# Optimization experiments

Measured on AMD Instinct MI355X. Metric: run time of the kernel, lower is better.

The kernel has to match this reference:

```python
import jax, jax.numpy as jnp
import numpy as np

N_NODES = 50000
N_EDGES = 400000
DIM = 64
HEADS = 8
NUM_GRAPHS = 64
OUT_DIM = 32
NEG_SLOPE = 0.2
EPS = 1e-5


def setup_inputs() -> dict:
    key = jax.random.key(0)
    ks = jax.random.split(key, 20)
    inp = {
        "x": jax.random.normal(ks[0], (N_NODES, DIM), dtype=jnp.float32),
        "edge_index": jax.random.randint(ks[1], (2, N_EDGES), 0, N_NODES, dtype=jnp.int64),
        "batch": jnp.sort(jax.random.randint(ks[2], (N_NODES,), 0, NUM_GRAPHS, dtype=jnp.int64)),
    }
    s = 0.05
    # GATConv layer 1 (in=DIM, out=DIM per head, heads=HEADS, concat=False)
    inp["W1"] = jax.random.normal(ks[3], (DIM, HEADS * DIM), dtype=jnp.float32) * s
    inp["a_src1"] = jax.random.normal(ks[4], (HEADS, DIM), dtype=jnp.float32) * s
    inp["a_dst1"] = jax.random.normal(ks[5], (HEADS, DIM), dtype=jnp.float32) * s
    inp["b1"] = jnp.zeros((DIM,), dtype=jnp.float32)
    inp["ln1_w"] = jnp.ones((DIM,), dtype=jnp.float32)
    inp["ln1_b"] = jnp.zeros((DIM,), dtype=jnp.float32)
    # GATConv layer 2
    inp["W2"] = jax.random.normal(ks[6], (DIM, HEADS * DIM), dtype=jnp.float32) * s
    inp["a_src2"] = jax.random.normal(ks[7], (HEADS, DIM), dtype=jnp.float32) * s
    inp["a_dst2"] = jax.random.normal(ks[8], (HEADS, DIM), dtype=jnp.float32) * s
    inp["b2"] = jnp.zeros((DIM,), dtype=jnp.float32)
    inp["ln2_w"] = jnp.ones((DIM,), dtype=jnp.float32)
    inp["ln2_b"] = jnp.zeros((DIM,), dtype=jnp.float32)
    # DownStream head
    inp["Wh"] = jax.random.normal(ks[9], (DIM, OUT_DIM), dtype=jnp.float32) * s
    inp["bh"] = jnp.zeros((OUT_DIM,), dtype=jnp.float32)
    return inp


def _edge_softmax(logits, dst, n):
    # per-destination-node softmax over incoming edges; logits: [E, H]
    m = jax.ops.segment_max(logits, dst, num_segments=n)
    e = jnp.exp(logits - m[dst])
    s = jax.ops.segment_sum(e, dst, num_segments=n)
    return e / (s[dst] + 1e-16)


def _gat_conv(x, src, dst, W, a_src, a_dst, b):
    # PyG GATConv, heads=HEADS, concat=False (mean over heads), eval mode (no dropout)
    n = x.shape[0]
    h = (x @ W).reshape(n, HEADS, -1)              # [N, H, D]
    al_s = jnp.einsum("nhd,hd->nh", h, a_src)      # [N, H]
    al_d = jnp.einsum("nhd,hd->nh", h, a_dst)
    logits = jax.nn.leaky_relu(al_s[src] + al_d[dst], NEG_SLOPE)  # [E, H]
    alpha = _edge_softmax(logits, dst, n)
    out = jax.ops.segment_sum(alpha[:, :, None] * h[src], dst, num_segments=n)  # [N, H, D]
    return out.mean(axis=1) + b


def _graph_layer_norm(x, batch, w, b):
    # PyG LayerNorm mode='graph': normalize over all nodes and channels of each graph
    f = x.shape[1]
    cnt = jax.ops.segment_sum(jnp.ones((x.shape[0],), x.dtype), batch, num_segments=NUM_GRAPHS)
    norm = jnp.clip(cnt, 1.0) * f
    mean = jax.ops.segment_sum(x.sum(axis=-1), batch, num_segments=NUM_GRAPHS) / norm
    xc = x - mean[batch][:, None]
    var = jax.ops.segment_sum((xc * xc).sum(axis=-1), batch, num_segments=NUM_GRAPHS) / norm
    out = xc * jax.lax.rsqrt(var + EPS)[batch][:, None]
    return out * w + b


def reference(x, edge_index, batch, W1, a_src1, a_dst1, b1, ln1_w, ln1_b,
              W2, a_src2, a_dst2, b2, ln2_w, ln2_b, Wh, bh):
    n = x.shape[0]
    loops = jnp.arange(n, dtype=edge_index.dtype)
    src = jnp.concatenate([edge_index[0], loops])   # add_self_loops (PyG default)
    dst = jnp.concatenate([edge_index[1], loops])

    # My_GATConv (dropout is identity in eval)
    h = x + _gat_conv(x, src, dst, W1, a_src1, a_dst1, b1)
    h = jax.nn.relu(_graph_layer_norm(h, batch, ln1_w, ln1_b))
    h = h + _gat_conv(h, src, dst, W2, a_src2, a_dst2, b2)
    h = jax.nn.relu(_graph_layer_norm(h, batch, ln2_w, ln2_b))

    # global_mean_pool over batch
    cnt = jax.ops.segment_sum(jnp.ones((n,), h.dtype), batch, num_segments=NUM_GRAPHS)
    pooled = jax.ops.segment_sum(h, batch, num_segments=NUM_GRAPHS) / jnp.clip(cnt, 1.0)[:, None]

    # DownStream head
    return jax.nn.relu(pooled @ Wh + bh)
```

## Files before the change

kernel.cpp:

```cpp
#include <hip/hip_runtime.h>
#include <math.h>

#define N_NODES 50000
#define N_EDGES 400000
#define E_TOT   (N_EDGES + N_NODES)
#define NG      64
#define NEG_SLOPE 0.2f

typedef __attribute__((ext_vector_type(8))) short bf16x8;
typedef __attribute__((ext_vector_type(4))) float f32x4;

__device__ __forceinline__ float lrelu(float x){ return x > 0.f ? x : NEG_SLOPE * x; }
__device__ __forceinline__ ushort f2bf(float f){
  union { float f; unsigned u; } v; v.f = f;
  unsigned r = v.u + 0x7FFFu + ((v.u >> 16) & 1u);
  return (ushort)(r >> 16);
}
__device__ __forceinline__ float bf2f(ushort u){
  return __uint_as_float(((unsigned)u) << 16);
}
__device__ __forceinline__ float bflo(unsigned u){ return __uint_as_float(u << 16); }
__device__ __forceinline__ float bfhi(unsigned u){ return __uint_as_float(u & 0xffff0000u); }

__device__ __forceinline__ void acc8(float* acc, uint4 w, float xv){
  acc[0] = fmaf(bflo(w.x), xv, acc[0]);
  acc[1] = fmaf(bfhi(w.x), xv, acc[1]);
  acc[2] = fmaf(bflo(w.y), xv, acc[2]);
  acc[3] = fmaf(bfhi(w.y), xv, acc[3]);
  acc[4] = fmaf(bflo(w.z), xv, acc[4]);
  acc[5] = fmaf(bfhi(w.z), xv, acc[5]);
  acc[6] = fmaf(bflo(w.w), xv, acc[6]);
  acc[7] = fmaf(bfhi(w.w), xv, acc[7]);
}

#define SETUP_PREP   (2048 + 2 * 32768)
#define SETUP_BOUNDS (SETUP_PREP + N_NODES + 1)
#define SETUP_TOTAL  (SETUP_BOUNDS + E_TOT)

__global__ void setup_kernel(const float* __restrict__ W1, const float* __restrict__ as1,
                             const float* __restrict__ ad1, const float* __restrict__ W2,
                             const float* __restrict__ as2, const float* __restrict__ ad2,
                             const int* __restrict__ batch, const int* __restrict__ ei,
                             float* __restrict__ wa1, float* __restrict__ wa2,
                             ushort* __restrict__ w1pT, ushort* __restrict__ w2pT,
                             int* __restrict__ gstart, int* __restrict__ counts){
  int idx = blockIdx.x * blockDim.x + threadIdx.x;
  if (idx < 2048){
    const float* W = (idx < 1024) ? W1 : W2;
    const float* asr = (idx < 1024) ? as1 : as2;
    const float* adr = (idx < 1024) ? ad1 : ad2;
    float* wa = (idx < 1024) ? wa1 : wa2;
    int i = idx & 1023;
    int k = i >> 4, c = i & 15;
    int h = c & 7;
    const float* a = (c < 8) ? asr : adr;
    float s = 0.f;
#pragma unroll
    for (int d = 0; d < 64; ++d) s = fmaf(W[k * 512 + h * 64 + d], a[h * 64 + d], s);
    wa[i] = s;
  } else if (idx < SETUP_PREP){
    int i = idx - 2048;
    const float* W = (i < 32768) ? W1 : W2;
    ushort* wpT = (i < 32768) ? w1pT : w2pT;
    i &= 32767;
    int j = i >> 9, k = i & 511;
    int h = k >> 6, d = k & 63;
    wpT[i] = f2bf(W[d * 512 + h * 64 + j] * 0.125f);
  } else if (idx < SETUP_BOUNDS){
    int n = idx - SETUP_PREP;
    int g = (n < N_NODES) ? batch[n] : NG;
    if (n == 0){
      for (int gg = 0; gg <= g; ++gg) gstart[gg] = 0;
    } else {
      int gp = batch[n - 1];
      for (int gg = gp + 1; gg <= g; ++gg) gstart[gg] = n;
    }
  } else if (idx < SETUP_TOTAL){
    int e = idx - SETUP_BOUNDS;
    int dst = (e < N_EDGES) ? ei[N_EDGES + e] : (e - N_EDGES);
    atomicAdd(&counts[dst], 1);
  }
}

#define SCAN_B 1024
#define SCAN_NB ((N_NODES + SCAN_B - 1) / SCAN_B)

__global__ __launch_bounds__(SCAN_B) void scan1_kernel(const int* __restrict__ counts,
                                                       int* __restrict__ row_off,
                                                       int* __restrict__ blocksum){
  __shared__ int sh[SCAN_B];
  int i = blockIdx.x * SCAN_B + threadIdx.x;
  int v = (i < N_NODES) ? counts[i] : 0;
  sh[threadIdx.x] = v;
  __syncthreads();
#pragma unroll
  for (int off = 1; off < SCAN_B; off <<= 1){
    int add = (threadIdx.x >= (unsigned)off) ? sh[threadIdx.x - off] : 0;
    __syncthreads();
    sh[threadIdx.x] += add;
    __syncthreads();
  }
  if (i < N_NODES) row_off[i] = sh[threadIdx.x] - v;
  if (threadIdx.x == SCAN_B - 1) blocksum[blockIdx.x] = sh[SCAN_B - 1];
}

__global__ void scan2_kernel(int* __restrict__ blocksum, int* __restrict__ blockoff){
  __shared__ int sh[64];
  int t = threadIdx.x;
  int v = (t < SCAN_NB) ? blocksum[t] : 0;
  sh[t] = v;
  __syncthreads();
#pragma unroll
  for (int off = 1; off < 64; off <<= 1){
    int add = (t >= off) ? sh[t - off] : 0;
    __syncthreads();
    sh[t] += add;
    __syncthreads();
  }
  if (t < SCAN_NB) blockoff[t] = sh[t] - v;
  if (t == 63) blockoff[SCAN_NB] = sh[63];
}

__global__ void scan3_kernel(int* __restrict__ row_off, const int* __restrict__ blockoff){
  int i = blockIdx.x * blockDim.x + threadIdx.x;
  if (i < N_NODES) row_off[i] += blockoff[i >> 10];
  if (i == 0) row_off[N_NODES] = blockoff[SCAN_NB];
}

__global__ void scatter_kernel(const int* __restrict__ ei, const int* __restrict__ row_off,
                               int* __restrict__ cursor, int* __restrict__ csr_src){
  int e = blockIdx.x * blockDim.x + threadIdx.x;
  if (e >= E_TOT) return;
  int src, dst;
  if (e < N_EDGES){ src = ei[e]; dst = ei[N_EDGES + e]; }
  else            { src = dst = e - N_EDGES; }
  int pos = row_off[dst] + atomicAdd(&cursor[dst], 1);
  csr_src[pos] = src;
}

__global__ void al1_kernel(const float* __restrict__ xin, const float* __restrict__ wa,
                           float* __restrict__ al, ushort* __restrict__ xbf){
  __shared__ float w[64 * 16];
  for (int i = threadIdx.x; i < 1024; i += blockDim.x) w[i] = wa[i];
  __syncthreads();
  int idx = blockIdx.x * blockDim.x + threadIdx.x;
  if (idx >= N_NODES * 16) return;
  int n = idx >> 4, c = idx & 15;
  const float* xr = xin + (size_t)n * 64;
  float s = 0.f;
#pragma unroll
  for (int k4 = 0; k4 < 16; ++k4){
    float4 v = *(const float4*)(xr + k4 * 4);
    s = fmaf(v.x, w[(k4 * 4 + 0) * 16 + c], s);
    s = fmaf(v.y, w[(k4 * 4 + 1) * 16 + c], s);
    s = fmaf(v.z, w[(k4 * 4 + 2) * 16 + c], s);
    s = fmaf(v.w, w[(k4 * 4 + 3) * 16 + c], s);
  }
  float4 mine = *(const float4*)(xr + c * 4);
  ushort ob[4] = {f2bf(mine.x), f2bf(mine.y), f2bf(mine.z), f2bf(mine.w)};
  *(ushort4*)(xbf + (size_t)n * 64 + c * 4) = *(const ushort4*)ob;
  al[idx] = s;
}

__global__ void al2_kernel(const ushort* __restrict__ xin, const float* __restrict__ wa,
                           float* __restrict__ al){
  __shared__ float w[64 * 16];
  for (int i = threadIdx.x; i < 1024; i += blockDim.x) w[i] = wa[i];
  __syncthreads();
  int idx = blockIdx.x * blockDim.x + threadIdx.x;
  if (idx >= N_NODES * 16) return;
  int n = idx >> 4, c = idx & 15;
  const ushort* xr = xin + (size_t)n * 64;
  float s = 0.f;
#pragma unroll
  for (int k8 = 0; k8 < 8; ++k8){
    uint4 u = *(const uint4*)(xr + k8 * 8);
    unsigned uu[4] = {u.x, u.y, u.z, u.w};
#pragma unroll
    for (int j = 0; j < 4; ++j){
      int k = k8 * 8 + j * 2;
      s = fmaf(bflo(uu[j]), w[k * 16 + c], s);
      s = fmaf(bfhi(uu[j]), w[(k + 1) * 16 + c], s);
    }
  }
  al[idx] = s;
}

__global__ __launch_bounds__(256) void wagg_kernel(const ushort* __restrict__ xb,
                                                   const float* __restrict__ al,
                                                   const int* __restrict__ row_off,
                                                   const int* __restrict__ csr_src,
                                                   ushort* __restrict__ aggx){
  __shared__ ushort ws[4][64][8];
  __shared__ int sdeg[4];
  const int wave = threadIdx.x >> 6, lane = threadIdx.x & 63;
  const int n = blockIdx.x * 4 + wave;
  const int s0 = row_off[n], s1 = row_off[n + 1];
  const int deg = s1 - s0;
  if (lane == 0) sdeg[wave] = deg;
  __syncthreads();
  const int mdeg = max(max(sdeg[0], sdeg[1]), max(sdeg[2], sdeg[3]));
  const int nchunk = (mdeg + 63) >> 6;

  const int eo = lane >> 3, h = lane & 7;
  const float ald = al[n * 16 + 8 + h];

  const bool fast = (deg <= 64);
  float wv[8];
  float sum = 0.f;
  if (fast){
#pragma unroll
    for (int i = 0; i < 8; ++i){
      int e = s0 + eo + i * 8;
      float v = 0.f;
      if (e < s1){ int s = csr_src[e]; v = __expf(lrelu(al[s * 16 + h] + ald)); }
      wv[i] = v; sum += v;
    }
  } else {
    for (int e = s0 + eo; e < s1; e += 8){
      int s = csr_src[e];
      sum += __expf(lrelu(al[s * 16 + h] + ald));
    }
  }
#pragma unroll
  for (int off = 8; off < 64; off <<= 1) sum += __shfl_xor(sum, off, 64);
  const float inv = 1.f / (sum + 1e-16f);

  float acc[8];
#pragma unroll
  for (int i = 0; i < 8; ++i) acc[i] = 0.f;

  for (int c = 0; c < nchunk; ++c){
    const int base = s0 + c * 64;
    if (fast){
      if (c == 0){
#pragma unroll
        for (int i = 0; i < 8; ++i){
          int e = s0 + eo + i * 8;
          if (e < s1) ws[wave][eo + i * 8][h] = f2bf(wv[i] * inv);
        }
      }
    } else {
#pragma unroll
      for (int i = 0; i < 8; ++i){
        int e = base + eo + i * 8;
        if (e < s1){
          int s = csr_src[e];
          ws[wave][e - base][h] = f2bf(__expf(lrelu(al[s * 16 + h] + ald)) * inv);
        }
      }
    }
    __syncthreads();
    const int cend = min(base + 64, s1);
    int e = base;
    for (; e + 4 <= cend; e += 4){
      int sa = csr_src[e], sb = csr_src[e + 1], sc = csr_src[e + 2], sd = csr_src[e + 3];
      float xa = bf2f(xb[(size_t)sa * 64 + lane]);
      float xc = bf2f(xb[(size_t)sb * 64 + lane]);
      float xe = bf2f(xb[(size_t)sc * 64 + lane]);
      float xg = bf2f(xb[(size_t)sd * 64 + lane]);
      uint4 wa = *(const uint4*)ws[wave][e - base];
      uint4 wb = *(const uint4*)ws[wave][e - base + 1];
      uint4 wc = *(const uint4*)ws[wave][e - base + 2];
      uint4 wd = *(const uint4*)ws[wave][e - base + 3];
      acc8(acc, wa, xa);
      acc8(acc, wb, xc);
      acc8(acc, wc, xe);
      acc8(acc, wd, xg);
    }
    for (; e < cend; ++e){
      int sa = csr_src[e];
      float xa = bf2f(xb[(size_t)sa * 64 + lane]);
      uint4 wa = *(const uint4*)ws[wave][e - base];
      acc8(acc, wa, xa);
    }
    __syncthreads();
  }
#pragma unroll
  for (int i = 0; i < 8; ++i)
    aggx[(size_t)n * 512 + i * 64 + lane] = f2bf(acc[i]);
}

__global__ __launch_bounds__(256) void outgemm_stats_kernel(const ushort* __restrict__ A,
                                                            const ushort* __restrict__ BT,
                                                            const float* __restrict__ bias,
                                                            const float* __restrict__ res,
                                                            const int* __restrict__ batch,
                                                            float* __restrict__ Y,
                                                            float* __restrict__ gs,
                                                            float* __restrict__ gss){
  __shared__ ushort Al[64][136];
  __shared__ ushort Bl[64][136];
  __shared__ float gsl[NG], gssl[NG];
  const int t = threadIdx.x;
  const int wave = t >> 6, lane = t & 63;
  const int rowbase = blockIdx.x * 64;
  const int frow = lane & 15, kc = lane >> 4;
  if (t < NG){ gsl[t] = 0.f; gssl[t] = 0.f; }
  f32x4 acc[4];
#pragma unroll
  for (int ct = 0; ct < 4; ++ct) acc[ct] = (f32x4){0.f, 0.f, 0.f, 0.f};

  for (int k0 = 0; k0 < 512; k0 += 128){
#pragma unroll
    for (int ppass = 0; ppass < 4; ++ppass){
      int idx = (ppass * 256 + t) * 8;
      int r = idx >> 7, k = idx & 127;
      int grow = rowbase + r;
      uint4 v = make_uint4(0u, 0u, 0u, 0u);
      if (grow < N_NODES) v = *(const uint4*)(A + (size_t)grow * 512 + k0 + k);
      *(uint4*)&Al[r][k] = v;
      uint4 w = *(const uint4*)(BT + (size_t)r * 512 + k0 + k);
      *(uint4*)&Bl[r][k] = w;
    }
    __syncthreads();
#pragma unroll
    for (int kf = 0; kf < 4; ++kf){
      bf16x8 a = *(const bf16x8*)&Al[wave * 16 + frow][kf * 32 + kc * 8];
#pragma unroll
      for (int ct = 0; ct < 4; ++ct){
        bf16x8 b = *(const bf16x8*)&Bl[ct * 16 + frow][kf * 32 + kc * 8];
        acc[ct] = __builtin_amdgcn_mfma_f32_16x16x32_bf16(a, b, acc[ct], 0, 0, 0);
      }
    }
    __syncthreads();
  }
  const int col0 = lane & 15, rsub = (lane >> 4) * 4;
  float rs[4] = {0.f, 0.f, 0.f, 0.f}, rss[4] = {0.f, 0.f, 0.f, 0.f};
#pragma unroll
  for (int ct = 0; ct < 4; ++ct){
    int col = ct * 16 + col0;
    float bs = bias[col];
#pragma unroll
    for (int j = 0; j < 4; ++j){
      int grow = rowbase + wave * 16 + rsub + j;
      if (grow < N_NODES){
        float y = acc[ct][j] + bs + res[(size_t)grow * 64 + col];
        Y[(size_t)grow * 64 + col] = y;
        rs[j] += y;
        rss[j] = fmaf(y, y, rss[j]);
      }
    }
  }
#pragma unroll
  for (int j = 0; j < 4; ++j){
#pragma unroll
    for (int off = 1; off < 16; off <<= 1){
      rs[j] += __shfl_xor(rs[j], off, 64);
      rss[j] += __shfl_xor(rss[j], off, 64);
    }
  }
  if (col0 == 0){
#pragma unroll
    for (int j = 0; j < 4; ++j){
      int grow = rowbase + wave * 16 + rsub + j;
      if (grow < N_NODES){
        int g = batch[grow];
        atomicAdd(&gsl[g], rs[j]);
        atomicAdd(&gssl[g], rss[j]);
      }
    }
  }
  __syncthreads();
  if (t < NG && (gsl[t] != 0.f || gssl[t] != 0.f)){
    atomicAdd(&gs[t], gsl[t]);
    atomicAdd(&gss[t], gssl[t]);
  }
}

__global__ void norm_relu_kernel(const float* __restrict__ Y, const int* __restrict__ batch,
                                 const int* __restrict__ gstart, const float* __restrict__ gs,
                                 const float* __restrict__ gss,
                                 const float* __restrict__ lw, const float* __restrict__ lb,
                                 float* __restrict__ out, ushort* __restrict__ outb){
  int idx = blockIdx.x * blockDim.x + threadIdx.x;
  if (idx >= N_NODES * 64) return;
  int n = idx >> 6, c = idx & 63;
  int g = batch[n];
  float cnt = (float)(gstart[g + 1] - gstart[g]);
  float norm = fmaxf(cnt, 1.f) * 64.f;
  float m = gs[g] / norm;
  float var = fmaxf(gss[g] / norm - m * m, 0.f);
  float rstd = rsqrtf(var + 1e-5f);
  float v = (Y[idx] - m) * rstd * lw[c] + lb[c];
  float r = fmaxf(v, 0.f);
  out[idx] = r;
  outb[idx] = f2bf(r);
}

__global__ void norm_relu_pool_kernel(const float* __restrict__ Y, const int* __restrict__ batch,
                                      const int* __restrict__ gstart, const float* __restrict__ gs,
                                      const float* __restrict__ gss,
                                      const float* __restrict__ lw, const float* __restrict__ lb,
                                      float* __restrict__ pooled){
  int w = (int)((blockIdx.x * blockDim.x + threadIdx.x) >> 6);
  int lane = threadIdx.x & 63;
  int nbase = w * 16;
  if (nbase >= N_NODES) return;
  int nend = min(nbase + 16, N_NODES);
  float accv = 0.f;
  int g = batch[nbase];
  float cnt = (float)(gstart[g + 1] - gstart[g]);
  float norm = fmaxf(cnt, 1.f) * 64.f;
  float m = gs[g] / norm;
  float var = fmaxf(gss[g] / norm - m * m, 0.f);
  float rstd = rsqrtf(var + 1e-5f);
  for (int n = nbase; n < nend; ++n){
    int gn = batch[n];
    if (gn != g){
      atomicAdd(&pooled[g * 64 + lane], accv);
      accv = 0.f; g = gn;
      cnt = (float)(gstart[g + 1] - gstart[g]);
      norm = fmaxf(cnt, 1.f) * 64.f;
      m = gs[g] / norm;
      var = fmaxf(gss[g] / norm - m * m, 0.f);
      rstd = rsqrtf(var + 1e-5f);
    }
    float v = (Y[(size_t)n * 64 + lane] - m) * rstd * lw[lane] + lb[lane];
    accv += fmaxf(v, 0.f);
  }
  atomicAdd(&pooled[g * 64 + lane], accv);
}

__global__ void head_kernel(const float* __restrict__ pooled, const int* __restrict__ gstart,
                            const float* __restrict__ Wh, const float* __restrict__ bh,
                            float* __restrict__ out){
  int idx = blockIdx.x * blockDim.x + threadIdx.x;
  if (idx >= NG * 32) return;
  int g = idx >> 5, o = idx & 31;
  float cnt = (float)(gstart[g + 1] - gstart[g]);
  float inv = 1.f / fmaxf(cnt, 1.f);
  float s = 0.f;
#pragma unroll
  for (int d = 0; d < 64; ++d) s = fmaf(pooled[g * 64 + d] * inv, Wh[d * 32 + o], s);
  out[idx] = fmaxf(s + bh[o], 0.f);
}

extern "C" void kernel_launch(void* const* d_in, const int* in_sizes, int n_in,
                              void* d_out, int out_size, void* d_ws, size_t ws_size,
                              hipStream_t stream){
  const float* x     = (const float*)d_in[0];
  const int*   ei    = (const int*)d_in[1];
  const int*   batch = (const int*)d_in[2];
  const float* W1    = (const float*)d_in[3];
  const float* as1   = (const float*)d_in[4];
  const float* ad1   = (const float*)d_in[5];
  const float* b1    = (const float*)d_in[6];
  const float* l1w   = (const float*)d_in[7];
  const float* l1b   = (const float*)d_in[8];
  const float* W2    = (const float*)d_in[9];
  const float* as2   = (const float*)d_in[10];
  const float* ad2   = (const float*)d_in[11];
  const float* b2    = (const float*)d_in[12];
  const float* l2w   = (const float*)d_in[13];
  const float* l2b   = (const float*)d_in[14];
  const float* Wh    = (const float*)d_in[15];
  const float* bh    = (const float*)d_in[16];
  float* out = (float*)d_out;

  char* p = (char*)d_ws;
  auto alloc = [&](size_t bytes) -> void* {
    void* r = (void*)p;
    p += (bytes + 255) & ~(size_t)255;
    return r;
  };
  int*    counts   = (int*)alloc(N_NODES * 4);
  int*    cursor   = (int*)alloc(N_NODES * 4);
  int*    row_off  = (int*)alloc((N_NODES + 1) * 4);
  int*    csr_src  = (int*)alloc(E_TOT * 4);
  int*    gstart   = (int*)alloc((NG + 1) * 4);
  int*    blocksum = (int*)alloc((SCAN_NB + 1) * 4);
  int*    blockoff = (int*)alloc((SCAN_NB + 1) * 4);
  float*  wa1      = (float*)alloc(64 * 16 * 4);
  float*  wa2      = (float*)alloc(64 * 16 * 4);
  ushort* w1pT     = (ushort*)alloc(64 * 512 * 2);
  ushort* w2pT     = (ushort*)alloc(64 * 512 * 2);
  float*  al       = (float*)alloc((size_t)N_NODES * 16 * 4);
  ushort* xbf      = (ushort*)alloc((size_t)N_NODES * 64 * 2);
  ushort* y1b      = (ushort*)alloc((size_t)N_NODES * 64 * 2);
  ushort* aggx     = (ushort*)alloc((size_t)N_NODES * 512 * 2);
  float*  y1p      = (float*)alloc((size_t)N_NODES * 64 * 4);
  float*  y1       = (float*)alloc((size_t)N_NODES * 64 * 4);
  float*  y2p      = y1p;
  float*  gstats   = (float*)alloc(8 * NG * 4);
  float*  pooled   = (float*)alloc(NG * 64 * 4);
  float* gs1 = gstats, *gss1 = gstats + NG, *gs2 = gstats + 2*NG, *gss2 = gstats + 3*NG;

  hipMemsetAsync(counts, 0, (size_t)((char*)row_off - (char*)counts), stream);
  hipMemsetAsync(gstats, 0, (size_t)((char*)pooled - (char*)gstats) + NG * 64 * 4, stream);

  setup_kernel<<<(SETUP_TOTAL + 255) / 256, 256, 0, stream>>>(
      W1, as1, ad1, W2, as2, ad2, batch, ei, wa1, wa2, w1pT, w2pT, gstart, counts);

  scan1_kernel<<<SCAN_NB, SCAN_B, 0, stream>>>(counts, row_off, blocksum);
  scan2_kernel<<<1, 64, 0, stream>>>(blocksum, blockoff);
  scan3_kernel<<<(N_NODES + 255) / 256, 256, 0, stream>>>(row_off, blockoff);
  scatter_kernel<<<(E_TOT + 255) / 256, 256, 0, stream>>>(ei, row_off, cursor, csr_src);

  const int waggBlocks = N_NODES / 4;
  const int waveBlocks = ((N_NODES + 15) / 16 * 64 + 255) / 256;
  const int gemmBlocks = (N_NODES + 63) / 64;

  al1_kernel<<<(N_NODES * 16 + 255) / 256, 256, 0, stream>>>(x, wa1, al, xbf);
  wagg_kernel<<<waggBlocks, 256, 0, stream>>>(xbf, al, row_off, csr_src, aggx);
  outgemm_stats_kernel<<<gemmBlocks, 256, 0, stream>>>(aggx, w1pT, b1, x, batch, y1p, gs1, gss1);
  norm_relu_kernel<<<(N_NODES * 64 + 255) / 256, 256, 0, stream>>>(y1p, batch, gstart, gs1, gss1, l1w, l1b, y1, y1b);

  al2_kernel<<<(N_NODES * 16 + 255) / 256, 256, 0, stream>>>(y1b, wa2, al);
  wagg_kernel<<<waggBlocks, 256, 0, stream>>>(y1b, al, row_off, csr_src, aggx);
  outgemm_stats_kernel<<<gemmBlocks, 256, 0, stream>>>(aggx, w2pT, b2, y1, batch, y2p, gs2, gss2);
  norm_relu_pool_kernel<<<waveBlocks, 256, 0, stream>>>(y2p, batch, gstart, gs2, gss2, l2w, l2b, pooled);

  head_kernel<<<(NG * 32 + 255) / 256, 256, 0, stream>>>(pooled, gstart, Wh, bh, out);
}
```

Baseline: 251.4 us.

## Fuse layer-2 attention logits into norm-relu and rework GAT aggregation layout

The separate al2 kernel is folded into the layer-1 norm/relu kernel, which now computes the per-node attention dot products from the fp32 rows held in shared memory. This removes one launch and a re-read of the bf16 activations. In the aggregation kernel, neighbor indices are loaded once per wave and broadcast with shuffles instead of being re-read from global memory. Attention weights are kept in fp32 in LDS rather than bf16. The aggregated output layout changes to head-minor (d*8+h), so each lane writes one 16-byte vector, and the transposed weight prep is reordered to match. The trade-off is double the LDS for the weights and a serial 64-step dot product done by only one wave per block in the fused kernel.

```diff
diff --git a/kernel.cpp b/kernel.cpp
--- a/kernel.cpp
+++ b/kernel.cpp
@@ -21,17 +21,6 @@
 }
 __device__ __forceinline__ float bflo(unsigned u){ return __uint_as_float(u << 16); }
 __device__ __forceinline__ float bfhi(unsigned u){ return __uint_as_float(u & 0xffff0000u); }
-
-__device__ __forceinline__ void acc8(float* acc, uint4 w, float xv){
-  acc[0] = fmaf(bflo(w.x), xv, acc[0]);
-  acc[1] = fmaf(bfhi(w.x), xv, acc[1]);
-  acc[2] = fmaf(bflo(w.y), xv, acc[2]);
-  acc[3] = fmaf(bfhi(w.y), xv, acc[3]);
-  acc[4] = fmaf(bflo(w.z), xv, acc[4]);
-  acc[5] = fmaf(bfhi(w.z), xv, acc[5]);
-  acc[6] = fmaf(bflo(w.w), xv, acc[6]);
-  acc[7] = fmaf(bfhi(w.w), xv, acc[7]);
-}
 
 #define SETUP_PREP   (2048 + 2 * 32768)
 #define SETUP_BOUNDS (SETUP_PREP + N_NODES + 1)
@@ -64,7 +53,7 @@
     ushort* wpT = (i < 32768) ? w1pT : w2pT;
     i &= 32767;
     int j = i >> 9, k = i & 511;
-    int h = k >> 6, d = k & 63;
+    int d = k >> 3, h = k & 7;
     wpT[i] = f2bf(W[d * 512 + h * 64 + j] * 0.125f);
   } else if (idx < SETUP_BOUNDS){
     int n = idx - SETUP_PREP;
@@ -162,36 +151,12 @@
   al[idx] = s;
 }
 
-__global__ void al2_kernel(const ushort* __restrict__ xin, const float* __restrict__ wa,
-                           float* __restrict__ al){
-  __shared__ float w[64 * 16];
-  for (int i = threadIdx.x; i < 1024; i += blockDim.x) w[i] = wa[i];
-  __syncthreads();
-  int idx = blockIdx.x * blockDim.x + threadIdx.x;
-  if (idx >= N_NODES * 16) return;
-  int n = idx >> 4, c = idx & 15;
-  const ushort* xr = xin + (size_t)n * 64;
-  float s = 0.f;
-#pragma unroll
-  for (int k8 = 0; k8 < 8; ++k8){
-    uint4 u = *(const uint4*)(xr + k8 * 8);
-    unsigned uu[4] = {u.x, u.y, u.z, u.w};
-#pragma unroll
-    for (int j = 0; j < 4; ++j){
-      int k = k8 * 8 + j * 2;
-      s = fmaf(bflo(uu[j]), w[k * 16 + c], s);
-      s = fmaf(bfhi(uu[j]), w[(k + 1) * 16 + c], s);
-    }
-  }
-  al[idx] = s;
-}
-
 __global__ __launch_bounds__(256) void wagg_kernel(const ushort* __restrict__ xb,
                                                    const float* __restrict__ al,
                                                    const int* __restrict__ row_off,
                                                    const int* __restrict__ csr_src,
                                                    ushort* __restrict__ aggx){
-  __shared__ ushort ws[4][64][8];
+  __shared__ float ws[4][64][8];
   __shared__ int sdeg[4];
   const int wave = threadIdx.x >> 6, lane = threadIdx.x & 63;
   const int n = blockIdx.x * 4 + wave;
@@ -205,15 +170,18 @@
   const int eo = lane >> 3, h = lane & 7;
   const float ald = al[n * 16 + 8 + h];
 
+  int idxv = (s0 + lane < s1) ? csr_src[s0 + lane] : 0;
+
   const bool fast = (deg <= 64);
   float wv[8];
   float sum = 0.f;
   if (fast){
 #pragma unroll
     for (int i = 0; i < 8; ++i){
-      int e = s0 + eo + i * 8;
+      int ee = eo + i * 8;
+      int s = __shfl(idxv, ee, 64);
       float v = 0.f;
-      if (e < s1){ int s = csr_src[e]; v = __expf(lrelu(al[s * 16 + h] + ald)); }
+      if (ee < deg) v = __expf(lrelu(al[s * 16 + h] + ald));
       wv[i] = v; sum += v;
     }
   } else {
@@ -236,8 +204,8 @@
       if (c == 0){
 #pragma unroll
         for (int i = 0; i < 8; ++i){
-          int e = s0 + eo + i * 8;
-          if (e < s1) ws[wave][eo + i * 8][h] = f2bf(wv[i] * inv);
+          int ee = eo + i * 8;
+          if (ee < deg) ws[wave][ee][h] = wv[i] * inv;
         }
       }
     } else {
@@ -246,7 +214,7 @@
         int e = base + eo + i * 8;
         if (e < s1){
           int s = csr_src[e];
-          ws[wave][e - base][h] = f2bf(__expf(lrelu(al[s * 16 + h] + ald)) * inv);
+          ws[wave][e - base][h] = __expf(lrelu(al[s * 16 + h] + ald)) * inv;
         }
       }
     }
@@ -254,31 +222,63 @@
     const int cend = min(base + 64, s1);
     int e = base;
     for (; e + 4 <= cend; e += 4){
-      int sa = csr_src[e], sb = csr_src[e + 1], sc = csr_src[e + 2], sd = csr_src[e + 3];
+      int r0 = e - base;
+      int sa, sb, sc, sd;
+      if (fast){
+        sa = __shfl(idxv, e - s0, 64);
+        sb = __shfl(idxv, e - s0 + 1, 64);
+        sc = __shfl(idxv, e - s0 + 2, 64);
+        sd = __shfl(idxv, e - s0 + 3, 64);
+      } else {
+        sa = csr_src[e]; sb = csr_src[e + 1]; sc = csr_src[e + 2]; sd = csr_src[e + 3];
+      }
       float xa = bf2f(xb[(size_t)sa * 64 + lane]);
       float xc = bf2f(xb[(size_t)sb * 64 + lane]);
       float xe = bf2f(xb[(size_t)sc * 64 + lane]);
       float xg = bf2f(xb[(size_t)sd * 64 + lane]);
-      uint4 wa = *(const uint4*)ws[wave][e - base];
-      uint4 wb = *(const uint4*)ws[wave][e - base + 1];
-      uint4 wc = *(const uint4*)ws[wave][e - base + 2];
-      uint4 wd = *(const uint4*)ws[wave][e - base + 3];
-      acc8(acc, wa, xa);
-      acc8(acc, wb, xc);
-      acc8(acc, wc, xe);
-      acc8(acc, wd, xg);
+      float4 wa0 = *(const float4*)&ws[wave][r0][0];
+      float4 wa1 = *(const float4*)&ws[wave][r0][4];
+      float4 wb0 = *(const float4*)&ws[wave][r0 + 1][0];
+      float4 wb1 = *(const float4*)&ws[wave][r0 + 1][4];
+      float4 wc0 = *(const float4*)&ws[wave][r0 + 2][0];
+      float4 wc1 = *(const float4*)&ws[wave][r0 + 2][4];
+      float4 wd0 = *(const float4*)&ws[wave][r0 + 3][0];
+      float4 wd1 = *(const float4*)&ws[wave][r0 + 3][4];
+      acc[0] = fmaf(wa0.x, xa, acc[0]); acc[1] = fmaf(wa0.y, xa, acc[1]);
+      acc[2] = fmaf(wa0.z, xa, acc[2]); acc[3] = fmaf(wa0.w, xa, acc[3]);
+      acc[4] = fmaf(wa1.x, xa, acc[4]); acc[5] = fmaf(wa1.y, xa, acc[5]);
+      acc[6] = fmaf(wa1.z, xa, acc[6]); acc[7] = fmaf(wa1.w, xa, acc[7]);
+      acc[0] = fmaf(wb0.x, xc, acc[0]); acc[1] = fmaf(wb0.y, xc, acc[1]);
+      acc[2] = fmaf(wb0.z, xc, acc[2]); acc[3] = fmaf(wb0.w, xc, acc[3]);
+      acc[4] = fmaf(wb1.x, xc, acc[4]); acc[5] = fmaf(wb1.y, xc, acc[5]);
+      acc[6] = fmaf(wb1.z, xc, acc[6]); acc[7] = fmaf(wb1.w, xc, acc[7]);
+      acc[0] = fmaf(wc0.x, xe, acc[0]); acc[1] = fmaf(wc0.y, xe, acc[1]);
+      acc[2] = fmaf(wc0.z, xe, acc[2]); acc[3] = fmaf(wc0.w, xe, acc[3]);
+      acc[4] = fmaf(wc1.x, xe, acc[4]); acc[5] = fmaf(wc1.y, xe, acc[5]);
+      acc[6] = fmaf(wc1.z, xe, acc[6]); acc[7] = fmaf(wc1.w, xe, acc[7]);
+      acc[0] = fmaf(wd0.x, xg, acc[0]); acc[1] = fmaf(wd0.y, xg, acc[1]);
+      acc[2] = fmaf(wd0.z, xg, acc[2]); acc[3] = fmaf(wd0.w, xg, acc[3]);
+      acc[4] = fmaf(wd1.x, xg, acc[4]); acc[5] = fmaf(wd1.y, xg, acc[5]);
+      acc[6] = fmaf(wd1.z, xg, acc[6]); acc[7] = fmaf(wd1.w, xg, acc[7]);
     }
     for (; e < cend; ++e){
-      int sa = csr_src[e];
+      int r0 = e - base;
+      int sa = fast ? __shfl(idxv, e - s0, 64) : csr_src[e];
       float xa = bf2f(xb[(size_t)sa * 64 + lane]);
-      uint4 wa = *(const uint4*)ws[wave][e - base];
-      acc8(acc, wa, xa);
-    }
-    __syncthreads();
-  }
-#pragma unroll
-  for (int i = 0; i < 8; ++i)
-    aggx[(size_t)n * 512 + i * 64 + lane] = f2bf(acc[i]);
+      float4 wa0 = *(const float4*)&ws[wave][r0][0];
+      float4 wa1 = *(const float4*)&ws[wave][r0][4];
+      acc[0] = fmaf(wa0.x, xa, acc[0]); acc[1] = fmaf(wa0.y, xa, acc[1]);
+      acc[2] = fmaf(wa0.z, xa, acc[2]); acc[3] = fmaf(wa0.w, xa, acc[3]);
+      acc[4] = fmaf(wa1.x, xa, acc[4]); acc[5] = fmaf(wa1.y, xa, acc[5]);
+      acc[6] = fmaf(wa1.z, xa, acc[6]); acc[7] = fmaf(wa1.w, xa, acc[7]);
+    }
+    __syncthreads();
+  }
+  uint o[4];
+#pragma unroll
+  for (int i = 0; i < 4; ++i)
+    o[i] = (uint)f2bf(acc[2 * i]) | ((uint)f2bf(acc[2 * i + 1]) << 16);
+  *(uint4*)(aggx + (size_t)n * 512 + lane * 8) = make_uint4(o[0], o[1], o[2], o[3]);
 }
 
 __global__ __launch_bounds__(256) void outgemm_stats_kernel(const ushort* __restrict__ A,
@@ -368,24 +368,40 @@
   }
 }
 
-__global__ void norm_relu_kernel(const float* __restrict__ Y, const int* __restrict__ batch,
-                                 const int* __restrict__ gstart, const float* __restrict__ gs,
-                                 const float* __restrict__ gss,
-                                 const float* __restrict__ lw, const float* __restrict__ lb,
-                                 float* __restrict__ out, ushort* __restrict__ outb){
-  int idx = blockIdx.x * blockDim.x + threadIdx.x;
-  if (idx >= N_NODES * 64) return;
-  int n = idx >> 6, c = idx & 63;
+__global__ __launch_bounds__(256) void norm_relu_al_kernel(const float* __restrict__ Y,
+                                                           const int* __restrict__ batch,
+                                                           const int* __restrict__ gstart,
+                                                           const float* __restrict__ gs,
+                                                           const float* __restrict__ gss,
+                                                           const float* __restrict__ lw,
+                                                           const float* __restrict__ lb,
+                                                           const float* __restrict__ wa,
+                                                           float* __restrict__ out,
+                                                           ushort* __restrict__ outb,
+                                                           float* __restrict__ al){
+  __shared__ float rows[4][64];
+  const int t = threadIdx.x;
+  const int nl = t >> 6, c = t & 63;
+  const int n = blockIdx.x * 4 + nl;
   int g = batch[n];
   float cnt = (float)(gstart[g + 1] - gstart[g]);
   float norm = fmaxf(cnt, 1.f) * 64.f;
   float m = gs[g] / norm;
   float var = fmaxf(gss[g] / norm - m * m, 0.f);
   float rstd = rsqrtf(var + 1e-5f);
-  float v = (Y[idx] - m) * rstd * lw[c] + lb[c];
+  float v = (Y[(size_t)n * 64 + c] - m) * rstd * lw[c] + lb[c];
   float r = fmaxf(v, 0.f);
-  out[idx] = r;
-  outb[idx] = f2bf(r);
+  out[(size_t)n * 64 + c] = r;
+  outb[(size_t)n * 64 + c] = f2bf(r);
+  rows[nl][c] = r;
+  __syncthreads();
+  if (t < 64){
+    int nn = t >> 4, cc = t & 15;
+    float s = 0.f;
+#pragma unroll
+    for (int k = 0; k < 64; ++k) s = fmaf(rows[nn][k], wa[k * 16 + cc], s);
+    al[(size_t)(blockIdx.x * 4 + nn) * 16 + cc] = s;
+  }
 }
 
 __global__ void norm_relu_pool_kernel(const float* __restrict__ Y, const int* __restrict__ batch,
@@ -504,9 +520,8 @@
   al1_kernel<<<(N_NODES * 16 + 255) / 256, 256, 0, stream>>>(x, wa1, al, xbf);
   wagg_kernel<<<waggBlocks, 256, 0, stream>>>(xbf, al, row_off, csr_src, aggx);
   outgemm_stats_kernel<<<gemmBlocks, 256, 0, stream>>>(aggx, w1pT, b1, x, batch, y1p, gs1, gss1);
-  norm_relu_kernel<<<(N_NODES * 64 + 255) / 256, 256, 0, stream>>>(y1p, batch, gstart, gs1, gss1, l1w, l1b, y1, y1b);
-
-  al2_kernel<<<(N_NODES * 16 + 255) / 256, 256, 0, stream>>>(y1b, wa2, al);
+  norm_relu_al_kernel<<<waggBlocks, 256, 0, stream>>>(y1p, batch, gstart, gs1, gss1, l1w, l1b, wa2, y1, y1b, al);
+
   wagg_kernel<<<waggBlocks, 256, 0, stream>>>(y1b, al, row_off, csr_src, aggx);
   outgemm_stats_kernel<<<gemmBlocks, 256, 0, stream>>>(aggx, w2pT, b2, y1, batch, y2p, gs2, gss2);
   norm_relu_pool_kernel<<<waveBlocks, 256, 0, stream>>>(y2p, batch, gstart, gs2, gss2, l2w, l2b, pooled);
```

After: 231.9 us. 1.08x faster.
